# Performance work log

Measured on AMD Instinct MI355X. Metric: run time of the kernel, lower is better.

## Reference

```python
import jax, jax.numpy as jnp
import numpy as np

HID = 1024
DEPTH = 2

def _rhn_layer(x, Win, bin_, Wh, bh, Wt, bt):
    # x: [B, T, in]; returns outputs [B, T, H]
    B = x.shape[0]
    h0 = jnp.zeros((B, HID), dtype=x.dtype)
    xt = jnp.swapaxes(x, 0, 1)  # [T, B, in]

    def step(h_prev, x_t):
        h = x_t @ Win + bin_
        for i in range(DEPTH):
            t_gate = jax.nn.sigmoid(h @ Wt[i] + bt[i])
            h_layer = jnp.tanh(h @ Wh[i] + bh[i])
            h = t_gate * h_layer + (1.0 - t_gate) * h
        h_new = h + h_prev
        return h_new, h_new

    _, outs = jax.lax.scan(step, h0, xt)  # [T, B, H]
    return jnp.swapaxes(outs, 0, 1)


def setup_inputs() -> dict:
    key = jax.random.key(0)
    ks = jax.random.split(key, 16)
    B, T, IN, H, OUT = 64, 256, 128, HID, 128
    s = lambda fan_in: 1.0 / np.sqrt(fan_in)
    d = {}
    d["x"] = jax.random.normal(ks[0], (B, T, IN), dtype=jnp.float32)
    # layer 0 (input_size=IN)
    d["l0_Win"] = jax.random.uniform(ks[1], (IN, H), minval=-s(IN), maxval=s(IN))
    d["l0_bin"] = jax.random.uniform(ks[2], (H,), minval=-s(IN), maxval=s(IN))
    d["l0_Wh"] = jax.random.uniform(ks[3], (DEPTH, H, H), minval=-s(H), maxval=s(H))
    d["l0_bh"] = jax.random.uniform(ks[4], (DEPTH, H), minval=-s(H), maxval=s(H))
    d["l0_Wt"] = jax.random.uniform(ks[5], (DEPTH, H, H), minval=-s(H), maxval=s(H))
    d["l0_bt"] = jax.random.uniform(ks[6], (DEPTH, H), minval=-s(H), maxval=s(H))
    # layer 1 (input_size=H)
    d["l1_Win"] = jax.random.uniform(ks[7], (H, H), minval=-s(H), maxval=s(H))
    d["l1_bin"] = jax.random.uniform(ks[8], (H,), minval=-s(H), maxval=s(H))
    d["l1_Wh"] = jax.random.uniform(ks[9], (DEPTH, H, H), minval=-s(H), maxval=s(H))
    d["l1_bh"] = jax.random.uniform(ks[10], (DEPTH, H), minval=-s(H), maxval=s(H))
    d["l1_Wt"] = jax.random.uniform(ks[11], (DEPTH, H, H), minval=-s(H), maxval=s(H))
    d["l1_bt"] = jax.random.uniform(ks[12], (DEPTH, H), minval=-s(H), maxval=s(H))
    # final fc
    d["fc_W"] = jax.random.uniform(ks[13], (H, OUT), minval=-s(H), maxval=s(H))
    d["fc_b"] = jax.random.uniform(ks[14], (OUT,), minval=-s(H), maxval=s(H))
    return d


def reference(x, l0_Win, l0_bin, l0_Wh, l0_bh, l0_Wt, l0_bt,
              l1_Win, l1_bin, l1_Wh, l1_bh, l1_Wt, l1_bt, fc_W, fc_b):
    out = _rhn_layer(x, l0_Win, l0_bin, l0_Wh, l0_bh, l0_Wt, l0_bt)
    out = _rhn_layer(out, l1_Win, l1_bin, l1_Wh, l1_bh, l1_Wt, l1_bt)
    # forecast_horizon = 1 -> last time step only
    out = out[:, -1:, :] @ fc_W + fc_b  # [B, 1, OUT]
    return out
```

## Files before the change

kernel.cpp:

```cpp
#include <hip/hip_runtime.h>

typedef unsigned short u16;
typedef unsigned int u32;
typedef __bf16 bf16x8 __attribute__((ext_vector_type(8)));
typedef float floatx4 __attribute__((ext_vector_type(4)));

#define HID 1024
#define BATCH 64
#define SEQ 256
#define INDIM 128
#define OUTDIM 128
#define MROWS (BATCH*SEQ)

__device__ __forceinline__ float b2f(u16 u) {
    union { u32 u; float f; } v; v.u = ((u32)u) << 16; return v.f;
}
__device__ __forceinline__ u16 f2b(float f) {
    union { float f; u32 u; } v; v.f = f;
    u32 x = v.u;
    x += 0x7fffu + ((x >> 16) & 1u);
    return (u16)(x >> 16);
}
__device__ __forceinline__ float sigm(float x) { return 1.f / (1.f + __expf(-x)); }
__device__ __forceinline__ float tanh_f(float x) { return 2.f / (1.f + __expf(-2.f * x)) - 1.f; }

__device__ __forceinline__ void gld16(const u16* g, u16* l) {
    __builtin_amdgcn_global_load_lds(
        (const __attribute__((address_space(1))) void*)g,
        (__attribute__((address_space(3))) void*)l, 16, 0, 0);
}

__global__ void detect_dtype(const u16* __restrict__ w, int* __restrict__ flag) {
    __shared__ int s;
    if (threadIdx.x == 0) s = 0;
    __syncthreads();
    int bad = 0;
    for (int i = threadIdx.x; i < 4096; i += 256) {
        int e = (w[i] >> 7) & 0xff;
        if (e >= 127) bad = 1;
    }
    if (bad) atomicOr(&s, 1);
    __syncthreads();
    if (threadIdx.x == 0) *flag = s;
}

__device__ __forceinline__ int is_fp32(const u16* probe) {
    const int lane = threadIdx.x & 63;
    const int e = (probe[lane * 7] >> 7) & 0xff;
    return __ballot(e >= 127) != 0ULL;
}

struct CvtList { const void* s[7]; u16* d[7]; int n[7]; };

__global__ void convert7(CvtList C, const int* __restrict__ flag) {
    const int fp32 = *flag;
    const int z = blockIdx.y;
    const int n = C.n[z];
    const int stride = gridDim.x * 256;
    for (int i = blockIdx.x * 256 + threadIdx.x; i < n; i += stride) {
        u16 o;
        if (fp32) o = f2b(((const float*)C.s[z])[i]);
        else      o = ((const u16*)C.s[z])[i];
        C.d[z][i] = o;
    }
}

struct TListO {
    const void* s[10];
    u16*        d[10];
    int         R[10];
    int         Cc[10];
    long        off[10];
};

__global__ void transpose10(TListO L, const int* __restrict__ flag) {
    const int fp32 = *flag;
    const int z = blockIdx.z;
    const void* src = L.s[z];
    u16*        dst = L.d[z];
    const int R  = L.R[z];
    const int Cc = L.Cc[z];
    const long zo = L.off[z];
    const int tr = blockIdx.y * 32, tc = blockIdx.x * 32;
    if (tr >= R || tc >= Cc) return;
    __align__(16) __shared__ u16 t[32][33];
    const int tx = threadIdx.x, ty = threadIdx.y;
#pragma unroll
    for (int i = 0; i < 4; ++i) {
        const int r = ty + i * 8;
        const long e = zo + (long)(tr + r) * Cc + tc + tx;
        u16 v;
        if (fp32) v = f2b(((const float*)src)[e]);
        else      v = ((const u16*)src)[e];
        t[r][tx] = v;
    }
    __syncthreads();
#pragma unroll
    for (int i = 0; i < 4; ++i) {
        const int r = ty + i * 8;
        dst[(size_t)(tc + r) * R + tr + tx] = t[tx][r];
    }
}

__device__ __forceinline__ void tile_swizzle(int& m0, int& n0) {
    const int lin = blockIdx.y * gridDim.x + blockIdx.x;
    const int xcd = lin & 7;
    const int loc = lin >> 3;
    m0 = (xcd * 16 + (loc & 15)) * 128;
    n0 = (loc >> 4) * 128;
}

__global__ __launch_bounds__(256, 2) void gemm128(
    const u16* __restrict__ A, const u16* __restrict__ BT,
    const u16* __restrict__ bias, u16* __restrict__ C,
    int M, int N, int K)
{
    __align__(16) __shared__ u16 As[128 * 64];
    __align__(16) __shared__ u16 Bs[128 * 64];

    const int tid  = threadIdx.x;
    const int lane = tid & 63;
    const int wid  = tid >> 6;
    const int wr   = wid >> 1;
    const int wc   = wid & 1;

    int m0, n0;
    tile_swizzle(m0, n0);

    floatx4 acc[4][4] = {};

    const int srow = lane >> 3;
    const int scol = 8 * ((lane & 7) ^ (lane >> 3));
    const int cb   = wid * 4;
    const u16* Ag[4]; const u16* Bg[4];
    u16 *Al[4], *Bl[4];
#pragma unroll
    for (int j = 0; j < 4; ++j) {
        const int c = cb + j;
        const int r = c * 8 + srow;
        Ag[j] = A  + (size_t)(m0 + r) * K + scol;
        Bg[j] = BT + (size_t)(n0 + r) * K + scol;
        Al[j] = As + c * 512;
        Bl[j] = Bs + c * 512;
    }

    const int quad = lane >> 4;
    const int l16  = lane & 15;
    const int swz  = l16 & 7;

    const int nk = K >> 6;
    for (int kt = 0; kt < nk; ++kt) {
        __syncthreads();
#pragma unroll
        for (int j = 0; j < 4; ++j) {
            gld16(Ag[j], Al[j]);  gld16(Bg[j], Bl[j]);
            Ag[j] += 64; Bg[j] += 64;
        }
        __syncthreads();

#pragma unroll
        for (int kk = 0; kk < 2; ++kk) {
            const int slot = ((kk * 4 + quad) ^ swz) * 8;
            bf16x8 af[4], bfr[4];
#pragma unroll
            for (int i = 0; i < 4; ++i) {
                af[i]  = *(const bf16x8*)(As + (wr * 64 + i * 16 + l16) * 64 + slot);
                bfr[i] = *(const bf16x8*)(Bs + (wc * 64 + i * 16 + l16) * 64 + slot);
            }
#pragma unroll
            for (int i = 0; i < 4; ++i)
#pragma unroll
                for (int j = 0; j < 4; ++j)
                    acc[i][j] = __builtin_amdgcn_mfma_f32_16x16x32_bf16(af[i], bfr[j], acc[i][j], 0, 0, 0);
        }
    }

#pragma unroll
    for (int i = 0; i < 4; ++i) {
        const int rowb = m0 + wr * 64 + i * 16 + quad * 4;
#pragma unroll
        for (int j = 0; j < 4; ++j) {
            const int col = n0 + wc * 64 + j * 16 + l16;
            const float bv = b2f(bias[col]);
#pragma unroll
            for (int r = 0; r < 4; ++r)
                C[(size_t)(rowb + r) * N + col] = f2b(acc[i][j][r] + bv);
        }
    }
}

__global__ __launch_bounds__(256, 2) void gemm_hw(
    const u16* __restrict__ A,
    const u16* __restrict__ WtT,
    const u16* __restrict__ WhT,
    const u16* __restrict__ bt, const u16* __restrict__ bh,
    u16* __restrict__ Hout,
    int M, int N, int K)
{
    __align__(16) __shared__ u16 As [128 * 64];
    __align__(16) __shared__ u16 Bts[128 * 64];
    __align__(16) __shared__ u16 Bhs[128 * 64];

    const int tid  = threadIdx.x;
    const int lane = tid & 63;
    const int wid  = tid >> 6;
    const int wr   = wid >> 1;
    const int wc   = wid & 1;

    int m0, n0;
    tile_swizzle(m0, n0);

    floatx4 acct[4][4] = {};
    floatx4 acch[4][4] = {};

    const int srow = lane >> 3;
    const int scol = 8 * ((lane & 7) ^ (lane >> 3));
    const int cb   = wid * 4;
    const u16* Ag[4]; const u16* Tg[4]; const u16* Hg[4];
    u16 *Al[4], *Tl[4], *Hl[4];
#pragma unroll
    for (int j = 0; j < 4; ++j) {
        const int c = cb + j;
        const int r = c * 8 + srow;
        Ag[j] = A   + (size_t)(m0 + r) * K + scol;
        Tg[j] = WtT + (size_t)(n0 + r) * K + scol;
        Hg[j] = WhT + (size_t)(n0 + r) * K + scol;
        Al[j] = As  + c * 512;
        Tl[j] = Bts + c * 512;
        Hl[j] = Bhs + c * 512;
    }

    const int quad = lane >> 4;
    const int l16  = lane & 15;
    const int swz  = l16 & 7;

    const int nk = K >> 6;
    for (int kt = 0; kt < nk; ++kt) {
        __syncthreads();
#pragma unroll
        for (int j = 0; j < 4; ++j) {
            gld16(Ag[j], Al[j]);  gld16(Tg[j], Tl[j]);  gld16(Hg[j], Hl[j]);
            Ag[j] += 64; Tg[j] += 64; Hg[j] += 64;
        }
        __syncthreads();

#pragma unroll
        for (int kk = 0; kk < 2; ++kk) {
            const int slot = ((kk * 4 + quad) ^ swz) * 8;
            bf16x8 af[4], btf[4], bhf[4];
#pragma unroll
            for (int i = 0; i < 4; ++i) {
                af[i]  = *(const bf16x8*)(As  + (wr * 64 + i * 16 + l16) * 64 + slot);
                btf[i] = *(const bf16x8*)(Bts + (wc * 64 + i * 16 + l16) * 64 + slot);
                bhf[i] = *(const bf16x8*)(Bhs + (wc * 64 + i * 16 + l16) * 64 + slot);
            }
#pragma unroll
            for (int i = 0; i < 4; ++i)
#pragma unroll
                for (int j = 0; j < 4; ++j) {
                    acct[i][j] = __builtin_amdgcn_mfma_f32_16x16x32_bf16(af[i], btf[j], acct[i][j], 0, 0, 0);
                    acch[i][j] = __builtin_amdgcn_mfma_f32_16x16x32_bf16(af[i], bhf[j], acch[i][j], 0, 0, 0);
                }
        }
    }

#pragma unroll
    for (int i = 0; i < 4; ++i) {
        const int rowb = m0 + wr * 64 + i * 16 + quad * 4;
#pragma unroll
        for (int j = 0; j < 4; ++j) {
            const int col = n0 + wc * 64 + j * 16 + l16;
            const float btv = b2f(bt[col]);
            const float bhv = b2f(bh[col]);
#pragma unroll
            for (int r = 0; r < 4; ++r) {
                const size_t idx = (size_t)(rowb + r) * N + col;
                const float hold = b2f(A[idx]);
                const float tg = sigm(acct[i][j][r] + btv);
                const float hl = tanh_f(acch[i][j][r] + bhv);
                Hout[idx] = f2b(hold + tg * (hl - hold));
            }
        }
    }
}

__global__ __launch_bounds__(256, 2) void gemm_hw_sum(
    const u16* __restrict__ A,
    const u16* __restrict__ WtT,
    const u16* __restrict__ WhT,
    const u16* __restrict__ bt, const u16* __restrict__ bh,
    float* __restrict__ hsum,
    int M, int N, int K)
{
    __align__(16) __shared__ u16 As [128 * 64];
    __align__(16) __shared__ u16 Bts[128 * 64];
    __align__(16) __shared__ u16 Bhs[128 * 64];

    const int tid  = threadIdx.x;
    const int lane = tid & 63;
    const int wid  = tid >> 6;
    const int wr   = wid >> 1;
    const int wc   = wid & 1;

    int m0, n0;
    tile_swizzle(m0, n0);

    floatx4 acct[4][4] = {};
    floatx4 acch[4][4] = {};

    const int srow = lane >> 3;
    const int scol = 8 * ((lane & 7) ^ (lane >> 3));
    const int cb   = wid * 4;
    const u16* Ag[4]; const u16* Tg[4]; const u16* Hg[4];
    u16 *Al[4], *Tl[4], *Hl[4];
#pragma unroll
    for (int j = 0; j < 4; ++j) {
        const int c = cb + j;
        const int r = c * 8 + srow;
        Ag[j] = A   + (size_t)(m0 + r) * K + scol;
        Tg[j] = WtT + (size_t)(n0 + r) * K + scol;
        Hg[j] = WhT + (size_t)(n0 + r) * K + scol;
        Al[j] = As  + c * 512;
        Tl[j] = Bts + c * 512;
        Hl[j] = Bhs + c * 512;
    }

    const int quad = lane >> 4;
    const int l16  = lane & 15;
    const int swz  = l16 & 7;

    const int nk = K >> 6;
    for (int kt = 0; kt < nk; ++kt) {
        __syncthreads();
#pragma unroll
        for (int j = 0; j < 4; ++j) {
            gld16(Ag[j], Al[j]);  gld16(Tg[j], Tl[j]);  gld16(Hg[j], Hl[j]);
            Ag[j] += 64; Tg[j] += 64; Hg[j] += 64;
        }
        __syncthreads();

#pragma unroll
        for (int kk = 0; kk < 2; ++kk) {
            const int slot = ((kk * 4 + quad) ^ swz) * 8;
            bf16x8 af[4], btf[4], bhf[4];
#pragma unroll
            for (int i = 0; i < 4; ++i) {
                af[i]  = *(const bf16x8*)(As  + (wr * 64 + i * 16 + l16) * 64 + slot);
                btf[i] = *(const bf16x8*)(Bts + (wc * 64 + i * 16 + l16) * 64 + slot);
                bhf[i] = *(const bf16x8*)(Bhs + (wc * 64 + i * 16 + l16) * 64 + slot);
            }
#pragma unroll
            for (int i = 0; i < 4; ++i)
#pragma unroll
                for (int j = 0; j < 4; ++j) {
                    acct[i][j] = __builtin_amdgcn_mfma_f32_16x16x32_bf16(af[i], btf[j], acct[i][j], 0, 0, 0);
                    acch[i][j] = __builtin_amdgcn_mfma_f32_16x16x32_bf16(af[i], bhf[j], acch[i][j], 0, 0, 0);
                }
        }
    }

    const int b = m0 >> 8;
#pragma unroll
    for (int j = 0; j < 4; ++j) {
        const int col = n0 + wc * 64 + j * 16 + l16;
        const float btv = b2f(bt[col]);
        const float bhv = b2f(bh[col]);
        float colsum = 0.f;
#pragma unroll
        for (int i = 0; i < 4; ++i) {
            const int rowb = m0 + wr * 64 + i * 16 + quad * 4;
#pragma unroll
            for (int r = 0; r < 4; ++r) {
                const size_t idx = (size_t)(rowb + r) * N + col;
                const float hold = b2f(A[idx]);
                const float tg = sigm(acct[i][j][r] + btv);
                const float hl = tanh_f(acch[i][j][r] + bhv);
                colsum += hold + tg * (hl - hold);
            }
        }
        colsum += __shfl_xor(colsum, 16, 64);
        colsum += __shfl_xor(colsum, 32, 64);
        if (quad == 0)
            atomicAdd(&hsum[(size_t)b * HID + col], colsum);
    }
}

__global__ void zero_hf(float* __restrict__ p) {
    p[blockIdx.x * 256 + threadIdx.x] = 0.f;
}

__global__ void cumsum_t(u16* g) {
    const int id = blockIdx.x * 256 + threadIdx.x;
    const int b = id >> 10, f = id & 1023;
    size_t base = (size_t)b * SEQ * HID + f;
    float acc = 0.f;
#pragma unroll 4
    for (int t = 0; t < SEQ; ++t) {
        size_t idx = base + (size_t)t * HID;
        acc += b2f(g[idx]);
        g[idx] = f2b(acc);
    }
}

__global__ void fc_final(const float* __restrict__ hf, const void* __restrict__ W,
                         const void* __restrict__ bias, void* __restrict__ out) {
    __shared__ float sh[HID];
    const int fp32 = is_fp32((const u16*)W);
    const int b = blockIdx.x, o = threadIdx.x;
    for (int k = o; k < HID; k += 128) sh[k] = hf[(size_t)b * HID + k];
    __syncthreads();
    float acc;
    if (fp32) {
        acc = ((const float*)bias)[o];
        for (int k = 0; k < HID; ++k)
            acc += sh[k] * ((const float*)W)[(size_t)k * OUTDIM + o];
        ((float*)out)[b * OUTDIM + o] = acc;
    } else {
        acc = b2f(((const u16*)bias)[o]);
        for (int k = 0; k < HID; ++k)
            acc += sh[k] * b2f(((const u16*)W)[(size_t)k * OUTDIM + o]);
        ((u16*)out)[b * OUTDIM + o] = f2b(acc);
    }
}

extern "C" void kernel_launch(void* const* d_in, const int* in_sizes, int n_in,
                              void* d_out, int out_size, void* d_ws, size_t ws_size,
                              hipStream_t stream) {
    const void* x      = d_in[0];
    const void* l0_Win = d_in[1];
    const void* l0_bin = d_in[2];
    const void* l0_Wh  = d_in[3];
    const void* l0_bh  = d_in[4];
    const void* l0_Wt  = d_in[5];
    const void* l0_bt  = d_in[6];
    const void* l1_Win = d_in[7];
    const void* l1_bin = d_in[8];
    const void* l1_Wh  = d_in[9];
    const void* l1_bh  = d_in[10];
    const void* l1_Wt  = d_in[11];
    const void* l1_bt  = d_in[12];
    const void* fc_W   = d_in[13];
    const void* fc_b   = d_in[14];

    char* ws = (char*)d_ws;
    u16* Pa = (u16*)(ws);
    u16* Pb = (u16*)(ws + 33554432);
    u16* xc = Pb;
    u16* tW = (u16*)(ws + 67108864);
    u16* tWin0 = tW;
    u16* tWt00 = tWin0 + 131072;
    u16* tWt01 = tWt00 + 1048576;
    u16* tWh00 = tWt01 + 1048576;
    u16* tWh01 = tWh00 + 1048576;
    u16* tWin1 = tWh01 + 1048576;
    u16* tWt10 = tWin1 + 1048576;
    u16* tWt11 = tWt10 + 1048576;
    u16* tWh10 = tWt11 + 1048576;
    u16* tWh11 = tWh10 + 1048576;
    u16* smallb = tWh11 + 1048576;
    u16* binc0 = smallb;
    u16* bhc0  = binc0 + 1024;
    u16* btc0  = bhc0 + 2048;
    u16* binc1 = btc0 + 2048;
    u16* bhc1  = binc1 + 1024;
    u16* btc1  = bhc1 + 2048;
    int* flag  = (int*)(btc1 + 2048);
    float* hfinal = (float*)Pb;

    detect_dtype<<<1, 256, 0, stream>>>((const u16*)l0_Wh, flag);

    const long DD = (long)HID * HID;
    TListO L;
    L.s[0] = l0_Win; L.d[0] = tWin0; L.R[0] = INDIM; L.Cc[0] = HID; L.off[0] = 0;
    L.s[1] = l0_Wt;  L.d[1] = tWt00; L.R[1] = HID;   L.Cc[1] = HID; L.off[1] = 0;
    L.s[2] = l0_Wt;  L.d[2] = tWt01; L.R[2] = HID;   L.Cc[2] = HID; L.off[2] = DD;
    L.s[3] = l0_Wh;  L.d[3] = tWh00; L.R[3] = HID;   L.Cc[3] = HID; L.off[3] = 0;
    L.s[4] = l0_Wh;  L.d[4] = tWh01; L.R[4] = HID;   L.Cc[4] = HID; L.off[4] = DD;
    L.s[5] = l1_Win; L.d[5] = tWin1; L.R[5] = HID;   L.Cc[5] = HID; L.off[5] = 0;
    L.s[6] = l1_Wt;  L.d[6] = tWt10; L.R[6] = HID;   L.Cc[6] = HID; L.off[6] = 0;
    L.s[7] = l1_Wt;  L.d[7] = tWt11; L.R[7] = HID;   L.Cc[7] = HID; L.off[7] = DD;
    L.s[8] = l1_Wh;  L.d[8] = tWh10; L.R[8] = HID;   L.Cc[8] = HID; L.off[8] = 0;
    L.s[9] = l1_Wh;  L.d[9] = tWh11; L.R[9] = HID;   L.Cc[9] = HID; L.off[9] = DD;
    transpose10<<<dim3(32, 32, 10), dim3(32, 8), 0, stream>>>(L, flag);

    CvtList C7;
    C7.s[0] = x;      C7.d[0] = xc;    C7.n[0] = MROWS * INDIM;
    C7.s[1] = l0_bin; C7.d[1] = binc0; C7.n[1] = HID;
    C7.s[2] = l0_bh;  C7.d[2] = bhc0;  C7.n[2] = 2 * HID;
    C7.s[3] = l0_bt;  C7.d[3] = btc0;  C7.n[3] = 2 * HID;
    C7.s[4] = l1_bin; C7.d[4] = binc1; C7.n[4] = HID;
    C7.s[5] = l1_bh;  C7.d[5] = bhc1;  C7.n[5] = 2 * HID;
    C7.s[6] = l1_bt;  C7.d[6] = btc1;  C7.n[6] = 2 * HID;
    convert7<<<dim3(512, 7), 256, 0, stream>>>(C7, flag);

    gemm128<<<dim3(8, 128), 256, 0, stream>>>(xc, tWin0, binc0, Pa, MROWS, HID, INDIM);
    gemm_hw<<<dim3(8, 128), 256, 0, stream>>>(Pa, tWt00, tWh00, btc0, bhc0, Pb, MROWS, HID, HID);
    gemm_hw<<<dim3(8, 128), 256, 0, stream>>>(Pb, tWt01, tWh01, btc0 + HID, bhc0 + HID, Pa, MROWS, HID, HID);
    cumsum_t<<<256, 256, 0, stream>>>(Pa);

    gemm128<<<dim3(8, 128), 256, 0, stream>>>(Pa, tWin1, binc1, Pb, MROWS, HID, HID);
    gemm_hw<<<dim3(8, 128), 256, 0, stream>>>(Pb, tWt10, tWh10, btc1, bhc1, Pa, MROWS, HID, HID);
    zero_hf<<<256, 256, 0, stream>>>(hfinal);
    gemm_hw_sum<<<dim3(8, 128), 256, 0, stream>>>(Pa, tWt11, tWh11, btc1 + HID, bhc1 + HID,
                                                  hfinal, MROWS, HID, HID);

    fc_final<<<64, 128, 0, stream>>>(hfinal, fc_W, fc_b, d_out);
}
```

Before: 518.9 us.

## Rewrite dual-gate highway GEMM with 8-wave 256x128 tiles and double-buffered LDS

```diff
diff --git a/kernel.cpp b/kernel.cpp
--- a/kernel.cpp
+++ b/kernel.cpp
@@ -28,6 +28,18 @@
     __builtin_amdgcn_global_load_lds(
         (const __attribute__((address_space(1))) void*)g,
         (__attribute__((address_space(3))) void*)l, 16, 0, 0);
+}
+
+__device__ __forceinline__ void bar_sync() {
+    asm volatile("" ::: "memory");
+    __builtin_amdgcn_s_barrier();
+    asm volatile("" ::: "memory");
+}
+template <int N>
+__device__ __forceinline__ void vm_bar() {
+    asm volatile("s_waitcnt vmcnt(%0)" :: "n"(N) : "memory");
+    __builtin_amdgcn_s_barrier();
+    asm volatile("" ::: "memory");
 }
 
 __global__ void detect_dtype(const u16* __restrict__ w, int* __restrict__ flag) {
@@ -110,6 +122,14 @@
     n0 = (loc >> 4) * 128;
 }
 
+__device__ __forceinline__ void tile_swizzle8(int& m0, int& n0) {
+    const int lin = blockIdx.x;
+    const int xcd = lin & 7;
+    const int loc = lin >> 3;
+    m0 = (xcd * 8 + (loc & 7)) * 256;
+    n0 = (loc >> 3) * 128;
+}
+
 __global__ __launch_bounds__(256, 2) void gemm128(
     const u16* __restrict__ A, const u16* __restrict__ BT,
     const u16* __restrict__ bias, u16* __restrict__ C,
@@ -189,7 +209,121 @@
     }
 }
 
-__global__ __launch_bounds__(256, 2) void gemm_hw(
+__device__ __forceinline__ void hw8_mainloop(
+    const u16* __restrict__ A, const u16* __restrict__ WtT, const u16* __restrict__ WhT,
+    int m0, int n0, int K,
+    floatx4 (&acct)[4][4], floatx4 (&acch)[4][4])
+{
+    __align__(16) __shared__ u16 lds[65536];
+
+    const int tid  = threadIdx.x;
+    const int lane = tid & 63;
+    const int wid  = tid >> 6;
+    const int wr   = wid >> 1;
+    const int wc   = wid & 1;
+
+    const int srow = lane >> 3;
+    const int scol = 8 * ((lane & 7) ^ srow);
+
+    const u16* Ag = A   + (size_t)(m0 + wid * 32 + srow) * K + scol;
+    const u16* Tg = WtT + (size_t)(n0 + wid * 16 + srow) * K + scol;
+    const u16* Hg = WhT + (size_t)(n0 + wid * 16 + srow) * K + scol;
+    const size_t K8 = (size_t)K * 8;
+
+    u16* dA = lds + wid * 2048;
+    u16* dT = lds + 16384 + wid * 1024;
+    u16* dH = lds + 24576 + wid * 1024;
+
+    const int quad = lane >> 4;
+    const int l16  = lane & 15;
+    const int swz  = l16 & 7;
+    const int s0 = (quad ^ swz) * 8;
+    const int s1 = ((4 + quad) ^ swz) * 8;
+    const int ra = wr * 64 + l16;
+    const int rb = wc * 64 + l16;
+
+    gld16(Ag,           dA);
+    gld16(Ag +     K8,  dA + 512);
+    gld16(Ag + 2 * K8,  dA + 1024);
+    gld16(Ag + 3 * K8,  dA + 1536);
+    gld16(Tg,           dT);
+    gld16(Tg +     K8,  dT + 512);
+    gld16(Hg,           dH);
+    gld16(Hg +     K8,  dH + 512);
+    Ag += 64; Tg += 64; Hg += 64;
+
+    const int nk = K >> 6;
+    for (int kt = 0; kt < nk; ++kt) {
+        const int  cur = kt & 1;
+        const int  nb  = (cur ^ 1) * 32768;
+        const bool pf  = (kt + 1 < nk);
+        const u16* Sa = lds + cur * 32768;
+        const u16* St = Sa + 16384;
+        const u16* Sh = Sa + 24576;
+
+        bf16x8 af[4], bq[4];
+
+        vm_bar<2>();
+        if (pf) { gld16(Ag, dA + nb); gld16(Ag + K8, dA + nb + 512); }
+#pragma unroll
+        for (int i = 0; i < 4; ++i) {
+            af[i] = *(const bf16x8*)(Sa + (ra + i * 16) * 64 + s0);
+            bq[i] = *(const bf16x8*)(St + (rb + i * 16) * 64 + s0);
+        }
+        __builtin_amdgcn_s_setprio(1);
+#pragma unroll
+        for (int i = 0; i < 4; ++i)
+#pragma unroll
+            for (int j = 0; j < 4; ++j)
+                acct[i][j] = __builtin_amdgcn_mfma_f32_16x16x32_bf16(af[i], bq[j], acct[i][j], 0, 0, 0);
+        __builtin_amdgcn_s_setprio(0);
+
+        if (pf) { vm_bar<2>(); gld16(Ag + 2 * K8, dA + nb + 1024); gld16(Ag + 3 * K8, dA + nb + 1536); }
+        else    { vm_bar<0>(); }
+#pragma unroll
+        for (int i = 0; i < 4; ++i)
+            bq[i] = *(const bf16x8*)(Sh + (rb + i * 16) * 64 + s0);
+        __builtin_amdgcn_s_setprio(1);
+#pragma unroll
+        for (int i = 0; i < 4; ++i)
+#pragma unroll
+            for (int j = 0; j < 4; ++j)
+                acch[i][j] = __builtin_amdgcn_mfma_f32_16x16x32_bf16(af[i], bq[j], acch[i][j], 0, 0, 0);
+        __builtin_amdgcn_s_setprio(0);
+
+        bar_sync();
+        if (pf) { gld16(Tg, dT + nb); gld16(Tg + K8, dT + nb + 512); }
+#pragma unroll
+        for (int i = 0; i < 4; ++i) {
+            af[i] = *(const bf16x8*)(Sa + (ra + i * 16) * 64 + s1);
+            bq[i] = *(const bf16x8*)(St + (rb + i * 16) * 64 + s1);
+        }
+        __builtin_amdgcn_s_setprio(1);
+#pragma unroll
+        for (int i = 0; i < 4; ++i)
+#pragma unroll
+            for (int j = 0; j < 4; ++j)
+                acct[i][j] = __builtin_amdgcn_mfma_f32_16x16x32_bf16(af[i], bq[j], acct[i][j], 0, 0, 0);
+        __builtin_amdgcn_s_setprio(0);
+
+        bar_sync();
+        if (pf) { gld16(Hg, dH + nb); gld16(Hg + K8, dH + nb + 512); }
+#pragma unroll
+        for (int i = 0; i < 4; ++i)
+            bq[i] = *(const bf16x8*)(Sh + (rb + i * 16) * 64 + s1);
+        __builtin_amdgcn_s_setprio(1);
+#pragma unroll
+        for (int i = 0; i < 4; ++i)
+#pragma unroll
+            for (int j = 0; j < 4; ++j)
+                acch[i][j] = __builtin_amdgcn_mfma_f32_16x16x32_bf16(af[i], bq[j], acch[i][j], 0, 0, 0);
+        __builtin_amdgcn_s_setprio(0);
+
+        Ag += 64; Tg += 64; Hg += 64;
+    }
+}
+
+__global__ __launch_bounds__(512, 2) void gemm_hw8(
     const u16* __restrict__ A,
     const u16* __restrict__ WtT,
     const u16* __restrict__ WhT,
@@ -197,72 +331,20 @@
     u16* __restrict__ Hout,
     int M, int N, int K)
 {
-    __align__(16) __shared__ u16 As [128 * 64];
-    __align__(16) __shared__ u16 Bts[128 * 64];
-    __align__(16) __shared__ u16 Bhs[128 * 64];
+    int m0, n0;
+    tile_swizzle8(m0, n0);
+
+    floatx4 acct[4][4] = {};
+    floatx4 acch[4][4] = {};
+    hw8_mainloop(A, WtT, WhT, m0, n0, K, acct, acch);
 
     const int tid  = threadIdx.x;
     const int lane = tid & 63;
     const int wid  = tid >> 6;
     const int wr   = wid >> 1;
     const int wc   = wid & 1;
-
-    int m0, n0;
-    tile_swizzle(m0, n0);
-
-    floatx4 acct[4][4] = {};
-    floatx4 acch[4][4] = {};
-
-    const int srow = lane >> 3;
-    const int scol = 8 * ((lane & 7) ^ (lane >> 3));
-    const int cb   = wid * 4;
-    const u16* Ag[4]; const u16* Tg[4]; const u16* Hg[4];
-    u16 *Al[4], *Tl[4], *Hl[4];
-#pragma unroll
-    for (int j = 0; j < 4; ++j) {
-        const int c = cb + j;
-        const int r = c * 8 + srow;
-        Ag[j] = A   + (size_t)(m0 + r) * K + scol;
-        Tg[j] = WtT + (size_t)(n0 + r) * K + scol;
-        Hg[j] = WhT + (size_t)(n0 + r) * K + scol;
-        Al[j] = As  + c * 512;
-        Tl[j] = Bts + c * 512;
-        Hl[j] = Bhs + c * 512;
-    }
-
     const int quad = lane >> 4;
     const int l16  = lane & 15;
-    const int swz  = l16 & 7;
-
-    const int nk = K >> 6;
-    for (int kt = 0; kt < nk; ++kt) {
-        __syncthreads();
-#pragma unroll
-        for (int j = 0; j < 4; ++j) {
-            gld16(Ag[j], Al[j]);  gld16(Tg[j], Tl[j]);  gld16(Hg[j], Hl[j]);
-            Ag[j] += 64; Tg[j] += 64; Hg[j] += 64;
-        }
-        __syncthreads();
-
-#pragma unroll
-        for (int kk = 0; kk < 2; ++kk) {
-            const int slot = ((kk * 4 + quad) ^ swz) * 8;
-            bf16x8 af[4], btf[4], bhf[4];
-#pragma unroll
-            for (int i = 0; i < 4; ++i) {
-                af[i]  = *(const bf16x8*)(As  + (wr * 64 + i * 16 + l16) * 64 + slot);
-                btf[i] = *(const bf16x8*)(Bts + (wc * 64 + i * 16 + l16) * 64 + slot);
-                bhf[i] = *(const bf16x8*)(Bhs + (wc * 64 + i * 16 + l16) * 64 + slot);
-            }
-#pragma unroll
-            for (int i = 0; i < 4; ++i)
-#pragma unroll
-                for (int j = 0; j < 4; ++j) {
-                    acct[i][j] = __builtin_amdgcn_mfma_f32_16x16x32_bf16(af[i], btf[j], acct[i][j], 0, 0, 0);
-                    acch[i][j] = __builtin_amdgcn_mfma_f32_16x16x32_bf16(af[i], bhf[j], acch[i][j], 0, 0, 0);
-                }
-        }
-    }
 
 #pragma unroll
     for (int i = 0; i < 4; ++i) {
@@ -284,7 +366,7 @@
     }
 }
 
-__global__ __launch_bounds__(256, 2) void gemm_hw_sum(
+__global__ __launch_bounds__(512, 2) void gemm_hw8_sum(
     const u16* __restrict__ A,
     const u16* __restrict__ WtT,
     const u16* __restrict__ WhT,
@@ -292,72 +374,20 @@
     float* __restrict__ hsum,
     int M, int N, int K)
 {
-    __align__(16) __shared__ u16 As [128 * 64];
-    __align__(16) __shared__ u16 Bts[128 * 64];
-    __align__(16) __shared__ u16 Bhs[128 * 64];
+    int m0, n0;
+    tile_swizzle8(m0, n0);
+
+    floatx4 acct[4][4] = {};
+    floatx4 acch[4][4] = {};
+    hw8_mainloop(A, WtT, WhT, m0, n0, K, acct, acch);
 
     const int tid  = threadIdx.x;
     const int lane = tid & 63;
     const int wid  = tid >> 6;
     const int wr   = wid >> 1;
     const int wc   = wid & 1;
-
-    int m0, n0;
-    tile_swizzle(m0, n0);
-
-    floatx4 acct[4][4] = {};
-    floatx4 acch[4][4] = {};
-
-    const int srow = lane >> 3;
-    const int scol = 8 * ((lane & 7) ^ (lane >> 3));
-    const int cb   = wid * 4;
-    const u16* Ag[4]; const u16* Tg[4]; const u16* Hg[4];
-    u16 *Al[4], *Tl[4], *Hl[4];
-#pragma unroll
-    for (int j = 0; j < 4; ++j) {
-        const int c = cb + j;
-        const int r = c * 8 + srow;
-        Ag[j] = A   + (size_t)(m0 + r) * K + scol;
-        Tg[j] = WtT + (size_t)(n0 + r) * K + scol;
-        Hg[j] = WhT + (size_t)(n0 + r) * K + scol;
-        Al[j] = As  + c * 512;
-        Tl[j] = Bts + c * 512;
-        Hl[j] = Bhs + c * 512;
-    }
-
     const int quad = lane >> 4;
     const int l16  = lane & 15;
-    const int swz  = l16 & 7;
-
-    const int nk = K >> 6;
-    for (int kt = 0; kt < nk; ++kt) {
-        __syncthreads();
-#pragma unroll
-        for (int j = 0; j < 4; ++j) {
-            gld16(Ag[j], Al[j]);  gld16(Tg[j], Tl[j]);  gld16(Hg[j], Hl[j]);
-            Ag[j] += 64; Tg[j] += 64; Hg[j] += 64;
-        }
-        __syncthreads();
-
-#pragma unroll
-        for (int kk = 0; kk < 2; ++kk) {
-            const int slot = ((kk * 4 + quad) ^ swz) * 8;
-            bf16x8 af[4], btf[4], bhf[4];
-#pragma unroll
-            for (int i = 0; i < 4; ++i) {
-                af[i]  = *(const bf16x8*)(As  + (wr * 64 + i * 16 + l16) * 64 + slot);
-                btf[i] = *(const bf16x8*)(Bts + (wc * 64 + i * 16 + l16) * 64 + slot);
-                bhf[i] = *(const bf16x8*)(Bhs + (wc * 64 + i * 16 + l16) * 64 + slot);
-            }
-#pragma unroll
-            for (int i = 0; i < 4; ++i)
-#pragma unroll
-                for (int j = 0; j < 4; ++j) {
-                    acct[i][j] = __builtin_amdgcn_mfma_f32_16x16x32_bf16(af[i], btf[j], acct[i][j], 0, 0, 0);
-                    acch[i][j] = __builtin_amdgcn_mfma_f32_16x16x32_bf16(af[i], bhf[j], acch[i][j], 0, 0, 0);
-                }
-        }
-    }
 
     const int b = m0 >> 8;
 #pragma unroll
@@ -494,15 +524,15 @@
     convert7<<<dim3(512, 7), 256, 0, stream>>>(C7, flag);
 
     gemm128<<<dim3(8, 128), 256, 0, stream>>>(xc, tWin0, binc0, Pa, MROWS, HID, INDIM);
-    gemm_hw<<<dim3(8, 128), 256, 0, stream>>>(Pa, tWt00, tWh00, btc0, bhc0, Pb, MROWS, HID, HID);
-    gemm_hw<<<dim3(8, 128), 256, 0, stream>>>(Pb, tWt01, tWh01, btc0 + HID, bhc0 + HID, Pa, MROWS, HID, HID);
+    gemm_hw8<<<512, 512, 0, stream>>>(Pa, tWt00, tWh00, btc0, bhc0, Pb, MROWS, HID, HID);
+    gemm_hw8<<<512, 512, 0, stream>>>(Pb, tWt01, tWh01, btc0 + HID, bhc0 + HID, Pa, MROWS, HID, HID);
     cumsum_t<<<256, 256, 0, stream>>>(Pa);
 
     gemm128<<<dim3(8, 128), 256, 0, stream>>>(Pa, tWin1, binc1, Pb, MROWS, HID, HID);
-    gemm_hw<<<dim3(8, 128), 256, 0, stream>>>(Pb, tWt10, tWh10, btc1, bhc1, Pa, MROWS, HID, HID);
+    gemm_hw8<<<512, 512, 0, stream>>>(Pb, tWt10, tWh10, btc1, bhc1, Pa, MROWS, HID, HID);
     zero_hf<<<256, 256, 0, stream>>>(hfinal);
-    gemm_hw_sum<<<dim3(8, 128), 256, 0, stream>>>(Pa, tWt11, tWh11, btc1 + HID, bhc1 + HID,
-                                                  hfinal, MROWS, HID, HID);
+    gemm_hw8_sum<<<512, 512, 0, stream>>>(Pa, tWt11, tWh11, btc1 + HID, bhc1 + HID,
+                                          hfinal, MROWS, HID, HID);
 
     fc_final<<<64, 128, 0, stream>>>(hfinal, fc_W, fc_b, d_out);
 }
```

Result: slower. 558.2 us (+7.6%).
